# Kernel optimization log

Measured on AMD Instinct MI355X. Metric: run time of the kernel, lower is better.

The kernel has to match this reference:

```python
import jax, jax.numpy as jnp
import numpy as np


def _idxct_last(x):
    """IDCT-like transform along the last axis (DREAMPlace idxct):
        y_u = sum_{k=0}^{N-1} x_k * cos(pi * k * (u + 0.5) / N)
    computed via the Makhoul FFT trick: phase-twiddle + length-N IFFT + even/odd reorder.
    """
    N = x.shape[-1]
    k = jnp.arange(N)
    # twiddle: exp(i*pi*k/(2N))  (this is what dct_cpp/dct_cuda precompute as expk)
    phase = jnp.exp(1j * jnp.pi * k.astype(jnp.float32) / (2.0 * N)).astype(jnp.complex64)
    z = x.astype(jnp.complex64) * phase
    # f_n = sum_k z_k exp(+i 2pi k n / N)  == N * ifft(z)
    v = jnp.real(jnp.fft.ifft(z, axis=-1)) * N
    half = (N + 1) // 2
    # de-interleave: y[2i] = v[i], y[2i+1] = v[N-1-i]
    y = jnp.zeros_like(x)
    y = y.at[..., 0::2].set(v[..., :half].astype(x.dtype))
    y = y.at[..., 1::2].set(jnp.flip(v[..., half:], axis=-1).astype(x.dtype))
    return y


def idcct2_math(x):
    """2D inverse discrete cosine-cosine transform (separable):
        y_{u,v} = sum_{p,q} x_{p,q} cos(pi p (u+0.5)/M) cos(pi q (v+0.5)/N)
    equivalent to idxct(idxct(x)^T)^T.
    """
    y = _idxct_last(x)                      # transform along last dim (N)
    y = _idxct_last(jnp.swapaxes(y, -1, -2))  # transform along first dim (M)
    return jnp.swapaxes(y, -1, -2)


def setup_inputs() -> dict:
    key = jax.random.key(0)
    M, N = 4096, 4096
    x = jax.random.normal(key, (M, N), dtype=jnp.float32)
    return {"x": x}


def reference(x):
    return idcct2_math(x)
```

## Files before the change

kernel.cpp:

```cpp
#include <hip/hip_runtime.h>
#include <hip/hip_bf16.h>

typedef unsigned short u16;
typedef u16 us4 __attribute__((ext_vector_type(4)));
typedef u16 us8 __attribute__((ext_vector_type(8)));
typedef __bf16 bf16x8 __attribute__((ext_vector_type(8)));
typedef float f32x4 __attribute__((ext_vector_type(4)));

#define NDIM 4096
#define HDIM 2048

__device__ __forceinline__ u16 bfbits(float f) {
    __hip_bfloat16 h = __float2bfloat16(f);
    return __builtin_bit_cast(u16, h);
}
__device__ __forceinline__ float bf2f(u16 b) {
    return __builtin_bit_cast(float, ((unsigned)b) << 16);
}

__device__ __forceinline__ void gload_lds16(const u16* g, u16* l) {
    __builtin_amdgcn_global_load_lds((__attribute__((address_space(1))) void*)g,
                                     (__attribute__((address_space(3))) void*)l,
                                     16, 0, 0);
}

__global__ __launch_bounds__(256) void k_gencos2(u16* __restrict__ Ce, u16* __restrict__ Co) {
    int idx = blockIdx.x * 256 + threadIdx.x;
    int u = idx >> 8;
    int k0 = (idx & 255) * 8;
    unsigned step = (unsigned)(2 * u + 1);
    us8 e, o;
#pragma unroll
    for (int i = 0; i < 8; ++i) {
        unsigned kk = (unsigned)(k0 + i);
        unsigned te = (2u * kk * step) & 16383u;
        unsigned to = ((2u * kk + 1u) * step) & 16383u;
        e[i] = bfbits(cosf((float)te * 3.8349519697141029e-4f));
        o[i] = bfbits(cosf((float)to * 3.8349519697141029e-4f));
    }
    *(us8*)&Ce[(size_t)idx * 8] = e;
    *(us8*)&Co[(size_t)idx * 8] = o;
}

__global__ __launch_bounds__(256) void k_transpose_split(const float* __restrict__ X,
                                                         u16* __restrict__ Xe,
                                                         u16* __restrict__ Xo) {
    __shared__ float tile[64][65];
    int b  = blockIdx.x;
    int bx = (b & 63) * 64;
    int by = (b >> 6) * 64;
    int t  = threadIdx.x;
    int lr = t >> 4, lc = (t & 15) * 4;
#pragma unroll
    for (int r = 0; r < 64; r += 16) {
        float4 v = *(const float4*)&X[(size_t)(by + lr + r) * NDIM + bx + lc];
        tile[lr + r][lc + 0] = v.x;
        tile[lr + r][lc + 1] = v.y;
        tile[lr + r][lc + 2] = v.z;
        tile[lr + r][lc + 3] = v.w;
    }
    __syncthreads();
    int jl = t >> 2;
    int s8 = (t & 3) * 8;
    us8 e, o;
#pragma unroll
    for (int i = 0; i < 8; ++i) {
        e[i] = bfbits(tile[2 * (s8 + i)][jl]);
        o[i] = bfbits(tile[2 * (s8 + i) + 1][jl]);
    }
    size_t base = (size_t)(bx + jl) * HDIM + (by >> 1) + s8;
    *(us8*)&Xe[base] = e;
    *(us8*)&Xo[base] = o;
}

__global__ __launch_bounds__(256) void k_bfly1(const u16* __restrict__ S,
                                               const u16* __restrict__ D,
                                               u16* __restrict__ We,
                                               u16* __restrict__ Wo) {
    int idx = blockIdx.x * 256 + threadIdx.x;
    int u  = idx >> 9;
    int j0 = (idx & 511) * 8;
    us8 s8 = *(const us8*)&S[(size_t)u * NDIM + j0];
    us8 d8 = *(const us8*)&D[(size_t)u * NDIM + j0];
    us4 et, ot, eb, ob;
#pragma unroll
    for (int i = 0; i < 4; ++i) {
        float se = bf2f(s8[2 * i]),     de = bf2f(d8[2 * i]);
        float so = bf2f(s8[2 * i + 1]), dd = bf2f(d8[2 * i + 1]);
        et[i] = bfbits(se + de);  eb[i] = bfbits(se - de);
        ot[i] = bfbits(so + dd);  ob[i] = bfbits(so - dd);
    }
    size_t ct = (size_t)u * HDIM + (j0 >> 1);
    size_t cb = (size_t)(NDIM - 1 - u) * HDIM + (j0 >> 1);
    *(us4*)&We[ct] = et;  *(us4*)&Wo[ct] = ot;
    *(us4*)&We[cb] = eb;  *(us4*)&Wo[cb] = ob;
}

__global__ __launch_bounds__(256) void k_bfly2(const u16* __restrict__ S2,
                                               const u16* __restrict__ D2,
                                               float* __restrict__ Y) {
    int idx = blockIdx.x * 256 + threadIdx.x;
    int i  = idx >> 8;
    int v0 = (idx & 255) * 8;
    us8 s8 = *(const us8*)&S2[(size_t)i * HDIM + v0];
    us8 d8 = *(const us8*)&D2[(size_t)i * HDIM + v0];
    float sum[8], dif[8];
#pragma unroll
    for (int t = 0; t < 8; ++t) {
        float s = bf2f(s8[t]), d = bf2f(d8[t]);
        sum[t] = s + d;  dif[t] = s - d;
    }
    f32x4 a0, a1, r0, r1;
#pragma unroll
    for (int w = 0; w < 4; ++w) {
        a0[w] = sum[w];  a1[w] = sum[w + 4];
        r0[w] = dif[7 - w];  r1[w] = dif[3 - w];
    }
    float* row = Y + (size_t)i * NDIM;
    *(f32x4*)&row[v0]        = a0;
    *(f32x4*)&row[v0 + 4]    = a1;
    *(f32x4*)&row[4088 - v0] = r0;
    *(f32x4*)&row[4092 - v0] = r1;
}

#define BAR() do { asm volatile("" ::: "memory"); __builtin_amdgcn_s_barrier(); \
                   asm volatile("" ::: "memory"); } while (0)
#define WAITV(N) asm volatile("s_waitcnt vmcnt(" #N ")" ::: "memory")

template <int NTK, int LOG_NTN>
__global__ __launch_bounds__(512, 2) void gemm256h(const u16* __restrict__ A0,
                                                   const u16* __restrict__ A1,
                                                   const u16* __restrict__ B0,
                                                   const u16* __restrict__ B1,
                                                   u16* __restrict__ out) {
    constexpr int KD  = NTK * 64;
    constexpr int NTN = 1 << LOG_NTN;
    constexpr int LDC = NTN * 256;
    constexpr int MTILES = 128 >> LOG_NTN;

    __shared__ u16 As[2 * 256 * 64];
    __shared__ u16 Bs[2 * 256 * 64];

    const int tid  = threadIdx.x;
    const int wave = tid >> 6;
    const int lane = tid & 63;

    const int bid = blockIdx.x;
    const int swz = (bid & 7) * 32 + (bid >> 3);
    const int half = swz >> 7;
    const int r    = swz & 127;
    const int bm   = (r >> LOG_NTN) * 256;
    const int bn   = (r & (NTN - 1)) * 256;

    const u16* A = half ? A1 : A0;
    const u16* B = half ? B1 : B0;
    u16* Cp = out + (size_t)half * MTILES * 256 * LDC;

    const int wr = wave >> 2;
    const int wc = wave & 3;

    const int srow = lane >> 3;
    const int scol = ((lane & 7) ^ srow) << 3;

    const int fr   = lane & 15;
    const int hi   = lane >> 4;
    const int slot0 = ((hi)     ^ (lane & 7)) << 3;
    const int slot1 = ((hi + 4) ^ (lane & 7)) << 3;
    const int aRow = (wr * 128 + fr) * 64;
    const int bRow = (wc * 64 + fr) * 64;


    f32x4 acc[8][4] = {};
    bf16x8 aR[4][2], b01[2][2], b23[2][2];

#define STAGE_A(TK, H, BOFF)                                                     \
    do {                                                                         \
        const int _tk = (TK) & (NTK - 1);                                        \
        _Pragma("unroll")                                                        \
        for (int q = 0; q < 2; ++q) {                                            \
            const int seg  = wave * 2 + q;                                       \
            const int row0 = (H) * 64 + (seg & 7) * 8 + (seg >> 3) * 128;        \
            const u16* _g = A + (size_t)(bm + row0 + srow) * KD + _tk * 64 + scol; \
            gload_lds16(_g, As + (BOFF) + row0 * 64 + lane * 8);                 \
        }                                                                        \
    } while (0)

#define STAGE_B(TK, H, BOFF)                                                     \
    do {                                                                         \
        const int _tk = (TK) & (NTK - 1);                                        \
        _Pragma("unroll")                                                        \
        for (int q = 0; q < 2; ++q) {                                            \
            const int seg  = wave * 2 + q;                                       \
            const int row0 = (H) * 32 + (seg & 3) * 8 + (seg >> 2) * 64;         \
            const u16* _g = B + (size_t)(bn + row0 + srow) * KD + _tk * 64 + scol; \
            gload_lds16(_g, Bs + (BOFF) + row0 * 64 + lane * 8);                 \
        }                                                                        \
    } while (0)

#define LOAD_A(MB, BOFF)                                                        \
    _Pragma("unroll")                                                           \
    for (int mm = 0; mm < 4; ++mm) {                                            \
        aR[mm][0] = __builtin_bit_cast(bf16x8, *(const us8*)(As + (BOFF) + aRow + ((MB) + mm) * 1024 + slot0)); \
        aR[mm][1] = __builtin_bit_cast(bf16x8, *(const us8*)(As + (BOFF) + aRow + ((MB) + mm) * 1024 + slot1)); \
    }

#define LOAD_B(DST, NB, BOFF)                                                   \
    _Pragma("unroll")                                                           \
    for (int nn = 0; nn < 2; ++nn) {                                            \
        DST[nn][0] = __builtin_bit_cast(bf16x8, *(const us8*)(Bs + (BOFF) + bRow + ((NB) + nn) * 1024 + slot0)); \
        DST[nn][1] = __builtin_bit_cast(bf16x8, *(const us8*)(Bs + (BOFF) + bRow + ((NB) + nn) * 1024 + slot1)); \
    }

#define MFMA_Q(MB, NB, BREG)                                                    \
    do {                                                                        \
        __builtin_amdgcn_s_setprio(1);                                          \
        _Pragma("unroll")                                                       \
        for (int mm = 0; mm < 4; ++mm)                                          \
            _Pragma("unroll")                                                   \
            for (int nn = 0; nn < 2; ++nn) {                                    \
                acc[(MB)+mm][(NB)+nn] = __builtin_amdgcn_mfma_f32_16x16x32_bf16(aR[mm][0], BREG[nn][0], acc[(MB)+mm][(NB)+nn], 0, 0, 0); \
                acc[(MB)+mm][(NB)+nn] = __builtin_amdgcn_mfma_f32_16x16x32_bf16(aR[mm][1], BREG[nn][1], acc[(MB)+mm][(NB)+nn], 0, 0, 0); \
            }                                                                   \
        __builtin_amdgcn_s_setprio(0);                                          \
    } while (0)

    STAGE_B(0, 0, 0);
    STAGE_A(0, 0, 0);
    STAGE_B(0, 1, 0);
    STAGE_A(0, 1, 0);
    STAGE_B(1, 0, 16384);
    STAGE_A(1, 0, 16384);
    STAGE_B(1, 1, 16384);
    WAITV(6);
    BAR();

    for (int t = 0; t < NTK; t += 2) {
        LOAD_A(0, 0);
        LOAD_B(b01, 0, 0);
        STAGE_A(t + 1, 1, 16384);
        BAR();
        MFMA_Q(0, 0, b01);
        BAR();
        LOAD_B(b23, 2, 0);
        STAGE_B(t + 2, 0, 0);
        BAR();
        MFMA_Q(0, 2, b23);
        BAR();
        LOAD_A(4, 0);
        STAGE_A(t + 2, 0, 0);
        BAR();
        MFMA_Q(4, 2, b23);
        BAR();
        STAGE_B(t + 2, 1, 0);
        BAR();
        MFMA_Q(4, 0, b01);
        WAITV(6);
        BAR();
        LOAD_A(0, 16384);
        LOAD_B(b01, 0, 16384);
        STAGE_A(t + 2, 1, 0);
        BAR();
        MFMA_Q(0, 0, b01);
        BAR();
        LOAD_B(b23, 2, 16384);
        STAGE_B(t + 3, 0, 16384);
        BAR();
        MFMA_Q(0, 2, b23);
        BAR();
        LOAD_A(4, 16384);
        STAGE_A(t + 3, 0, 16384);
        BAR();
        MFMA_Q(4, 2, b23);
        BAR();
        STAGE_B(t + 3, 1, 16384);
        BAR();
        MFMA_Q(4, 0, b01);
        WAITV(6);
        BAR();
    }

    asm volatile("s_waitcnt vmcnt(0)" ::: "memory");

    const int orow0 = wr * 128 + hi * 4;
    const int ocol0 = bn + wc * 64 + fr;
#pragma unroll
    for (int m = 0; m < 8; ++m)
#pragma unroll
        for (int n = 0; n < 4; ++n) {
            f32x4 v = acc[m][n];
#pragma unroll
            for (int rr = 0; rr < 4; ++rr) {
                size_t off = (size_t)(bm + orow0 + m * 16 + rr) * LDC + (ocol0 + n * 16);
                Cp[off] = bfbits(v[rr]);
            }
        }
#undef STAGE_A
#undef STAGE_B
#undef LOAD_A
#undef LOAD_B
#undef MFMA_Q
}

extern "C" void kernel_launch(void* const* d_in, const int* in_sizes, int n_in,
                              void* d_out, int out_size, void* d_ws, size_t ws_size,
                              hipStream_t stream) {
    const float* X = (const float*)d_in[0];
    float* Y = (float*)d_out;

    const size_t QM = (size_t)HDIM * HDIM;
    u16* Ce = (u16*)d_ws;
    u16* Co = Ce + QM;
    u16* Xe = Co + QM;
    u16* Xo = Xe + 2 * QM;
    u16* S  = Xo + 2 * QM;
    u16* D  = S + 2 * QM;
    u16* We = Xe;
    u16* Wo = Xo;
    u16* S2 = S;
    u16* D2 = D;

    k_gencos2<<<2048, 256, 0, stream>>>(Ce, Co);
    k_transpose_split<<<4096, 256, 0, stream>>>(X, Xe, Xo);
    gemm256h<32, 4><<<256, 512, 0, stream>>>(Ce, Co, Xe, Xo, S);
    k_bfly1<<<4096, 256, 0, stream>>>(S, D, We, Wo);
    gemm256h<32, 3><<<256, 512, 0, stream>>>(We, Wo, Ce, Co, S2);
    k_bfly2<<<4096, 256, 0, stream>>>(S2, D2, Y);
}
```

Before: 174.3 us.

## Restructure GEMM inner loop to split K-slices and prefetch LDS reads across MFMA phases

```diff
diff --git a/kernel.cpp b/kernel.cpp
--- a/kernel.cpp
+++ b/kernel.cpp
@@ -169,9 +169,8 @@
     const int aRow = (wr * 128 + fr) * 64;
     const int bRow = (wc * 64 + fr) * 64;
 
-
     f32x4 acc[8][4] = {};
-    bf16x8 aR[4][2], b01[2][2], b23[2][2];
+    bf16x8 a0r[4], a1r[4], bb0[4], bb1[4];
 
 #define STAGE_A(TK, H, BOFF)                                                     \
     do {                                                                         \
@@ -197,30 +196,24 @@
         }                                                                        \
     } while (0)
 
-#define LOAD_A(MB, BOFF)                                                        \
+#define RD_A(DST, MB, SL, BOFF)                                                 \
     _Pragma("unroll")                                                           \
-    for (int mm = 0; mm < 4; ++mm) {                                            \
-        aR[mm][0] = __builtin_bit_cast(bf16x8, *(const us8*)(As + (BOFF) + aRow + ((MB) + mm) * 1024 + slot0)); \
-        aR[mm][1] = __builtin_bit_cast(bf16x8, *(const us8*)(As + (BOFF) + aRow + ((MB) + mm) * 1024 + slot1)); \
-    }
-
-#define LOAD_B(DST, NB, BOFF)                                                   \
+    for (int mm = 0; mm < 4; ++mm)                                              \
+        DST[mm] = __builtin_bit_cast(bf16x8, *(const us8*)(As + (BOFF) + aRow + ((MB) + mm) * 1024 + (SL)));
+
+#define RD_B(DST, SL, BOFF)                                                     \
     _Pragma("unroll")                                                           \
-    for (int nn = 0; nn < 2; ++nn) {                                            \
-        DST[nn][0] = __builtin_bit_cast(bf16x8, *(const us8*)(Bs + (BOFF) + bRow + ((NB) + nn) * 1024 + slot0)); \
-        DST[nn][1] = __builtin_bit_cast(bf16x8, *(const us8*)(Bs + (BOFF) + bRow + ((NB) + nn) * 1024 + slot1)); \
-    }
-
-#define MFMA_Q(MB, NB, BREG)                                                    \
+    for (int nn = 0; nn < 4; ++nn)                                              \
+        DST[nn] = __builtin_bit_cast(bf16x8, *(const us8*)(Bs + (BOFF) + bRow + nn * 1024 + (SL)));
+
+#define MFMA16(MB, AREG, BREG)                                                  \
     do {                                                                        \
         __builtin_amdgcn_s_setprio(1);                                          \
         _Pragma("unroll")                                                       \
         for (int mm = 0; mm < 4; ++mm)                                          \
             _Pragma("unroll")                                                   \
-            for (int nn = 0; nn < 2; ++nn) {                                    \
-                acc[(MB)+mm][(NB)+nn] = __builtin_amdgcn_mfma_f32_16x16x32_bf16(aR[mm][0], BREG[nn][0], acc[(MB)+mm][(NB)+nn], 0, 0, 0); \
-                acc[(MB)+mm][(NB)+nn] = __builtin_amdgcn_mfma_f32_16x16x32_bf16(aR[mm][1], BREG[nn][1], acc[(MB)+mm][(NB)+nn], 0, 0, 0); \
-            }                                                                   \
+            for (int nn = 0; nn < 4; ++nn)                                      \
+                acc[(MB)+mm][nn] = __builtin_amdgcn_mfma_f32_16x16x32_bf16(AREG[mm], BREG[nn], acc[(MB)+mm][nn], 0, 0, 0); \
         __builtin_amdgcn_s_setprio(0);                                          \
     } while (0)
 
@@ -233,49 +226,55 @@
     STAGE_B(1, 1, 16384);
     WAITV(6);
     BAR();
+    RD_A(a0r, 0, slot0, 0);
+    RD_B(bb0, slot0, 0);
 
     for (int t = 0; t < NTK; t += 2) {
-        LOAD_A(0, 0);
-        LOAD_B(b01, 0, 0);
         STAGE_A(t + 1, 1, 16384);
         BAR();
-        MFMA_Q(0, 0, b01);
-        BAR();
-        LOAD_B(b23, 2, 0);
+        MFMA16(0, a0r, bb0);
+        RD_A(a1r, 4, slot0, 0);
+        RD_B(bb1, slot1, 0);
+        BAR();
         STAGE_B(t + 2, 0, 0);
         BAR();
-        MFMA_Q(0, 2, b23);
-        BAR();
-        LOAD_A(4, 0);
+        MFMA16(4, a1r, bb0);
+        RD_A(a0r, 0, slot1, 0);
+        BAR();
         STAGE_A(t + 2, 0, 0);
         BAR();
-        MFMA_Q(4, 2, b23);
+        MFMA16(0, a0r, bb1);
+        RD_A(a1r, 4, slot1, 0);
         BAR();
         STAGE_B(t + 2, 1, 0);
         BAR();
-        MFMA_Q(4, 0, b01);
+        MFMA16(4, a1r, bb1);
         WAITV(6);
-        BAR();
-        LOAD_A(0, 16384);
-        LOAD_B(b01, 0, 16384);
+        RD_A(a0r, 0, slot0, 16384);
+        RD_B(bb0, slot0, 16384);
+        BAR();
         STAGE_A(t + 2, 1, 0);
         BAR();
-        MFMA_Q(0, 0, b01);
-        BAR();
-        LOAD_B(b23, 2, 16384);
+        MFMA16(0, a0r, bb0);
+        RD_A(a1r, 4, slot0, 16384);
+        RD_B(bb1, slot1, 16384);
+        BAR();
         STAGE_B(t + 3, 0, 16384);
         BAR();
-        MFMA_Q(0, 2, b23);
-        BAR();
-        LOAD_A(4, 16384);
+        MFMA16(4, a1r, bb0);
+        RD_A(a0r, 0, slot1, 16384);
+        BAR();
         STAGE_A(t + 3, 0, 16384);
         BAR();
-        MFMA_Q(4, 2, b23);
+        MFMA16(0, a0r, bb1);
+        RD_A(a1r, 4, slot1, 16384);
         BAR();
         STAGE_B(t + 3, 1, 16384);
         BAR();
-        MFMA_Q(4, 0, b01);
+        MFMA16(4, a1r, bb1);
         WAITV(6);
+        RD_A(a0r, 0, slot0, 0);
+        RD_B(bb0, slot0, 0);
         BAR();
     }
 
@@ -296,9 +295,9 @@
         }
 #undef STAGE_A
 #undef STAGE_B
-#undef LOAD_A
-#undef LOAD_B
-#undef MFMA_Q
+#undef RD_A
+#undef RD_B
+#undef MFMA16
 }
 
 extern "C" void kernel_launch(void* const* d_in, const int* in_sizes, int n_in,
```

Result: slower. 189.5 us (+8.7%).
